# Kernel tuning notes

Measured on AMD Instinct MI355X. Metric: run time of the kernel, lower is better.

The kernel has to match this reference:

```python
import jax, jax.numpy as jnp
import numpy as np

N_NODES = 100000
N_EDGES = 1600000
N_GRAPHS = 4096
HID = 512
OUT_DIM = 12


def setup_inputs() -> dict:
    key = jax.random.key(0)
    ks = jax.random.split(key, 16)
    x = jax.random.normal(ks[0], (N_NODES, 7), dtype=jnp.float32)
    edge_index = jax.random.randint(ks[1], (2, N_EDGES), 0, N_NODES, dtype=jnp.int32)
    batch = jnp.sort(jax.random.randint(ks[2], (N_NODES,), 0, N_GRAPHS, dtype=jnp.int32))

    def lin(k, i, o):
        s = 1.0 / np.sqrt(i)
        kw, kb = jax.random.split(k)
        return (jax.random.uniform(kw, (i, o), jnp.float32, -s, s),
                jax.random.uniform(kb, (o,), jnp.float32, -s, s))

    c1_w1, c1_b1 = lin(ks[3], 7, HID)
    c1_w2, c1_b2 = lin(ks[4], HID, HID)
    c2_w1, c2_b1 = lin(ks[5], HID, HID)
    c2_w2, c2_b2 = lin(ks[6], HID, HID)
    c3_w1, c3_b1 = lin(ks[7], HID, HID)
    c3_w2, c3_b2 = lin(ks[8], HID, HID)
    lin_w1, lin_b1 = lin(ks[9], HID, 256)
    lin_w2, lin_b2 = lin(ks[10], 256, OUT_DIM)
    return dict(x=x, edge_index=edge_index, batch=batch,
                c1_w1=c1_w1, c1_b1=c1_b1, c1_w2=c1_w2, c1_b2=c1_b2,
                c2_w1=c2_w1, c2_b1=c2_b1, c2_w2=c2_w2, c2_b2=c2_b2,
                c3_w1=c3_w1, c3_b1=c3_b1, c3_w2=c3_w2, c3_b2=c3_b2,
                lin_w1=lin_w1, lin_b1=lin_b1, lin_w2=lin_w2, lin_b2=lin_b2)


def _gin_conv(x, src, dst, w1, b1, w2, b2):
    # GINConv (eps=0): h_i = mlp(x_i + sum_{j in N(i)} x_j)
    agg = jax.ops.segment_sum(x[src], dst, num_segments=N_NODES)
    h = x + agg
    h = jax.nn.relu(h @ w1 + b1) @ w2 + b2
    return h


def reference(x, edge_index, batch,
              c1_w1, c1_b1, c1_w2, c1_b2,
              c2_w1, c2_b1, c2_w2, c2_b2,
              c3_w1, c3_b1, c3_w2, c3_b2,
              lin_w1, lin_b1, lin_w2, lin_b2):
    src, dst = edge_index[0], edge_index[1]
    h = jax.nn.relu(_gin_conv(x, src, dst, c1_w1, c1_b1, c1_w2, c1_b2))
    h = jax.nn.relu(_gin_conv(h, src, dst, c2_w1, c2_b1, c2_w2, c2_b2))
    h = jax.nn.relu(_gin_conv(h, src, dst, c3_w1, c3_b1, c3_w2, c3_b2))
    # global mean pool over graphs in batch
    sums = jax.ops.segment_sum(h, batch, num_segments=N_GRAPHS)
    cnts = jax.ops.segment_sum(jnp.ones((h.shape[0],), h.dtype), batch, num_segments=N_GRAPHS)
    pooled = sums / jnp.maximum(cnts, 1.0)[:, None]
    return jax.nn.relu(pooled @ lin_w1 + lin_b1) @ lin_w2 + lin_b2
```

## Files before the change

kernel.cpp:

```cpp
#include <hip/hip_runtime.h>
#include <hip/hip_bf16.h>
#include <cstddef>
#include <cstdint>

#define N_NODES   100000
#define M_PAD     100096
#define N_EDGES   1600000
#define N_GRAPHS  4096
#define HID       512
#define OUT_DIM   12

typedef unsigned short u16;
typedef __attribute__((ext_vector_type(8))) short bf16x8;
typedef __attribute__((ext_vector_type(4))) float f32x4;

__device__ inline float bf2f(u16 u) {
    union { uint32_t i; float f; } v; v.i = (uint32_t)u << 16; return v.f;
}
__device__ inline u16 f2bf(float f) {
    union { float f; uint32_t i; } v; v.f = f;
    uint32_t r = v.i + 0x7FFFu + ((v.i >> 16) & 1u);
    return (u16)(r >> 16);
}

__device__ inline void load8_bf(const u16* p, float o[8]) {
    uint4 u = *(const uint4*)p;
    uint32_t w[4] = {u.x, u.y, u.z, u.w};
    #pragma unroll
    for (int i = 0; i < 4; ++i) {
        o[2*i]   = bf2f((u16)(w[i] & 0xFFFFu));
        o[2*i+1] = bf2f((u16)(w[i] >> 16));
    }
}
__device__ inline void store8_bf(u16* p, const float o[8]) {
    uint4 u;
    u.x = (uint32_t)f2bf(o[0]) | ((uint32_t)f2bf(o[1]) << 16);
    u.y = (uint32_t)f2bf(o[2]) | ((uint32_t)f2bf(o[3]) << 16);
    u.z = (uint32_t)f2bf(o[4]) | ((uint32_t)f2bf(o[5]) << 16);
    u.w = (uint32_t)f2bf(o[6]) | ((uint32_t)f2bf(o[7]) << 16);
    *(uint4*)p = u;
}

__device__ inline void gld16(const void* g, void* l) {
    __builtin_amdgcn_global_load_lds(
        (const __attribute__((address_space(1))) void*)g,
        (__attribute__((address_space(3))) void*)(uint32_t)(uintptr_t)l,
        16, 0, 0);
}

__global__ void zero_ints(int* __restrict__ p, int n) {
    int i = blockIdx.x * blockDim.x + threadIdx.x;
    if (i < n) p[i] = 0;
}

__global__ void hist_kernel(const int* __restrict__ dst, int* __restrict__ counts) {
    int e = blockIdx.x * blockDim.x + threadIdx.x;
    if (e < N_EDGES) atomicAdd(&counts[dst[e]], 1);
}

#define SCAN_NB 98

__global__ __launch_bounds__(1024) void scan_chunks(const int* __restrict__ counts,
                                                    int* __restrict__ row_start,
                                                    int* __restrict__ partials) {
    __shared__ int smem[1024];
    int tid = threadIdx.x;
    int i = blockIdx.x * 1024 + tid;
    int v = (i < N_NODES) ? counts[i] : 0;
    smem[tid] = v;
    __syncthreads();
    for (int off = 1; off < 1024; off <<= 1) {
        int t = (tid >= off) ? smem[tid - off] : 0;
        __syncthreads();
        smem[tid] += t;
        __syncthreads();
    }
    if (i < N_NODES) row_start[i + 1] = smem[tid];
    if (tid == 1023) partials[blockIdx.x] = smem[1023];
}

__global__ void scan_partials(int* __restrict__ partials) {
    if (threadIdx.x == 0 && blockIdx.x == 0) {
        int run = 0;
        for (int b = 0; b < SCAN_NB; ++b) {
            int t = partials[b];
            partials[b] = run;
            run += t;
        }
    }
}

__global__ __launch_bounds__(1024) void scan_add_offsets(int* __restrict__ row_start,
                                                         const int* __restrict__ partials) {
    int i = blockIdx.x * 1024 + threadIdx.x;
    if (i == 0) row_start[0] = 0;
    if (i < N_NODES) row_start[i + 1] += partials[blockIdx.x];
}

__global__ void cursor_init(const int* __restrict__ row_start, int* __restrict__ cursor) {
    int i = blockIdx.x * blockDim.x + threadIdx.x;
    if (i < N_NODES) cursor[i] = row_start[i];
}

__global__ void scatter_edges(const int* __restrict__ src, const int* __restrict__ dst,
                              int* __restrict__ cursor, int* __restrict__ sorted_src) {
    int e = blockIdx.x * blockDim.x + threadIdx.x;
    if (e < N_EDGES) {
        int p = atomicAdd(&cursor[dst[e]], 1);
        p = min(max(p, 0), N_EDGES - 1);
        sorted_src[p] = src[e];
    }
}

__global__ __launch_bounds__(256) void transpose_to_bf16(const float* __restrict__ W,
                                                         u16* __restrict__ Wt) {
    __shared__ float t[32][33];
    int bx = blockIdx.x * 32, by = blockIdx.y * 32;
    int tx = threadIdx.x & 31, ty = threadIdx.x >> 5;
    #pragma unroll
    for (int i = 0; i < 32; i += 8)
        t[ty + i][tx] = W[(size_t)(by + ty + i) * HID + bx + tx];
    __syncthreads();
    #pragma unroll
    for (int i = 0; i < 32; i += 8)
        Wt[(size_t)(bx + ty + i) * HID + by + tx] = f2bf(t[tx][ty + i]);
}

template <int HALF>
__global__ __launch_bounds__(256) void agg_half(const u16* __restrict__ X,
                                                const int* __restrict__ row_start,
                                                const int* __restrict__ sorted_src,
                                                u16* __restrict__ Out) {
    int node = blockIdx.x * 4 + (threadIdx.x >> 6);
    int lane = threadIdx.x & 63;
    size_t col = HALF * 256 + lane * 4;
    uint2 s = *(const uint2*)(X + (size_t)node * HID + col);
    float a0 = bf2f((u16)(s.x & 0xFFFFu)), a1 = bf2f((u16)(s.x >> 16));
    float a2 = bf2f((u16)(s.y & 0xFFFFu)), a3 = bf2f((u16)(s.y >> 16));
    int e0 = min(row_start[node], N_EDGES);
    int e1 = min(row_start[node + 1], N_EDGES);
    for (int e = e0; e < e1; ++e) {
        unsigned si = min((unsigned)sorted_src[e], (unsigned)(N_NODES - 1));
        uint2 v = *(const uint2*)(X + (size_t)si * HID + col);
        a0 += bf2f((u16)(v.x & 0xFFFFu)); a1 += bf2f((u16)(v.x >> 16));
        a2 += bf2f((u16)(v.y & 0xFFFFu)); a3 += bf2f((u16)(v.y >> 16));
    }
    uint2 o;
    o.x = (uint32_t)f2bf(a0) | ((uint32_t)f2bf(a1) << 16);
    o.y = (uint32_t)f2bf(a2) | ((uint32_t)f2bf(a3) << 16);
    unsigned long long packed = (unsigned long long)o.x | ((unsigned long long)o.y << 32);
    __builtin_nontemporal_store(packed,
        (unsigned long long*)(Out + (size_t)node * HID + col));
}

__global__ __launch_bounds__(64) void agg7_kernel(const float* __restrict__ x,
                                                  const int* __restrict__ row_start,
                                                  const int* __restrict__ sorted_src,
                                                  float* __restrict__ out) {
    int node = blockIdx.x * 8 + (threadIdx.x >> 3);
    int d = threadIdx.x & 7;
    if (node >= N_NODES || d >= 7) return;
    float acc = x[(size_t)node * 7 + d];
    int e0 = min(row_start[node], N_EDGES);
    int e1 = min(row_start[node + 1], N_EDGES);
    for (int e = e0; e < e1; ++e) {
        unsigned si = min((unsigned)sorted_src[e], (unsigned)(N_NODES - 1));
        acc += x[(size_t)si * 7 + d];
    }
    out[(size_t)node * 7 + d] = acc;
}

__global__ __launch_bounds__(256) void gemm_k7_relu(const float* __restrict__ A7,
                                                    const float* __restrict__ W,
                                                    const float* __restrict__ bias,
                                                    u16* __restrict__ C) {
    __shared__ float Wl[7 * HID];
    __shared__ float Bi[HID];
    __shared__ float A7l[128 * 7];
    int tid = threadIdx.x;
    int node0 = blockIdx.x * 128;
    for (int t = tid; t < 7 * HID; t += 256) Wl[t] = W[t];
    for (int t = tid; t < HID; t += 256) Bi[t] = bias[t];
    for (int t = tid; t < 128 * 7; t += 256) {
        int gi = node0 * 7 + t;
        A7l[t] = (gi < N_NODES * 7) ? A7[gi] : 0.f;
    }
    __syncthreads();
    int wid = tid >> 6, lane = tid & 63;
    for (int it = 0; it < 32; ++it) {
        int nl = it * 4 + wid;
        int node = node0 + nl;
        if (node >= N_NODES) break;
        float a[7];
        #pragma unroll
        for (int k = 0; k < 7; ++k) a[k] = A7l[nl * 7 + k];
        float s[8];
        int c0 = lane * 8;
        #pragma unroll
        for (int c = 0; c < 8; ++c) {
            float v = Bi[c0 + c];
            #pragma unroll
            for (int k = 0; k < 7; ++k) v = fmaf(a[k], Wl[k * HID + c0 + c], v);
            s[c] = fmaxf(v, 0.f);
        }
        store8_bf(C + (size_t)node * HID + c0, s);
    }
}

template <bool RELU>
__global__ __launch_bounds__(256) void gemm_mfma_bf16(const u16* __restrict__ A,
                                                      const u16* __restrict__ Wt,
                                                      const float* __restrict__ bias,
                                                      u16* __restrict__ C) {
    __shared__ u16 As[128][32];
    __shared__ u16 Bs[128][32];
    const int tid  = threadIdx.x;
    const int wid  = tid >> 6;
    const int lane = tid & 63;
    const int wr = wid >> 1, wc = wid & 1;
    const int row0 = blockIdx.y * 128;
    const int col0 = blockIdx.x * 128;
    const int l15 = lane & 15;
    const int l4  = lane >> 4;

    const int srow = lane >> 2;
    const int scol = (lane & 3) * 8;

    f32x4 acc[4][4] = {};

    for (int k0 = 0; k0 < HID; k0 += 32) {
        const u16* Ag = A  + (size_t)(row0 + wid * 32) * HID + k0;
        const u16* Bg = Wt + (size_t)(col0 + wid * 32) * HID + k0;
        #pragma unroll
        for (int i = 0; i < 2; ++i) {
            gld16(Ag + (size_t)(i * 16 + srow) * HID + scol, &As[wid * 32 + i * 16][0]);
            gld16(Bg + (size_t)(i * 16 + srow) * HID + scol, &Bs[wid * 32 + i * 16][0]);
        }
        __syncthreads();
        bf16x8 af[4], bfr[4];
        #pragma unroll
        for (int m = 0; m < 4; ++m)
            af[m] = *(const bf16x8*)&As[wr * 64 + m * 16 + l15][l4 * 8];
        #pragma unroll
        for (int n = 0; n < 4; ++n)
            bfr[n] = *(const bf16x8*)&Bs[wc * 64 + n * 16 + l15][l4 * 8];
        #pragma unroll
        for (int m = 0; m < 4; ++m)
            #pragma unroll
            for (int n = 0; n < 4; ++n)
                acc[m][n] = __builtin_amdgcn_mfma_f32_16x16x32_bf16(af[m], bfr[n],
                                                                    acc[m][n], 0, 0, 0);
        __syncthreads();
    }

    #pragma unroll
    for (int m = 0; m < 4; ++m) {
        #pragma unroll
        for (int n = 0; n < 4; ++n) {
            int col = col0 + wc * 64 + n * 16 + l15;
            float b = bias[col];
            #pragma unroll
            for (int i = 0; i < 4; ++i) {
                int r = row0 + wr * 64 + m * 16 + l4 * 4 + i;
                float v = acc[m][n][i] + b;
                if (RELU) v = fmaxf(v, 0.f);
                C[(size_t)r * HID + col] = f2bf(v);
            }
        }
    }
}

template <bool RELU>
__global__ __launch_bounds__(256) void gemm_tiled_f32(const float* __restrict__ A,
                                                      const float* __restrict__ W,
                                                      const float* __restrict__ bias,
                                                      float* __restrict__ C,
                                                      int M, int N, int K) {
    __shared__ float As[16][68];
    __shared__ float Bs[16][68];
    int tid = threadIdx.x;
    int tx = tid & 15, ty = tid >> 4;
    int col0 = blockIdx.x * 64;
    int row0 = blockIdx.y * 64;
    float acc[4][4] = {};

    for (int k0 = 0; k0 < K; k0 += 16) {
        {
            int r = tid >> 2, c = (tid & 3) * 4;
            float4 v = make_float4(0.f, 0.f, 0.f, 0.f);
            int gr = row0 + r;
            if (gr < M) v = *reinterpret_cast<const float4*>(A + (size_t)gr * K + k0 + c);
            As[c + 0][r] = v.x; As[c + 1][r] = v.y; As[c + 2][r] = v.z; As[c + 3][r] = v.w;
        }
        {
            int r = tid >> 4, c = (tid & 15) * 4;
            int gc = col0 + c;
            float4 v = make_float4(0.f, 0.f, 0.f, 0.f);
            const float* wp = W + (size_t)(k0 + r) * N + gc;
            if (gc + 3 < N) {
                v = *reinterpret_cast<const float4*>(wp);
            } else {
                float t0 = (gc + 0 < N) ? wp[0] : 0.f;
                float t1 = (gc + 1 < N) ? wp[1] : 0.f;
                float t2 = (gc + 2 < N) ? wp[2] : 0.f;
                v = make_float4(t0, t1, t2, 0.f);
            }
            *reinterpret_cast<float4*>(&Bs[r][c]) = v;
        }
        __syncthreads();
        #pragma unroll
        for (int k = 0; k < 16; ++k) {
            float a[4], b[4];
            *(float4*)a = *(const float4*)&As[k][ty * 4];
            *(float4*)b = *(const float4*)&Bs[k][tx * 4];
            #pragma unroll
            for (int i = 0; i < 4; ++i)
                #pragma unroll
                for (int j = 0; j < 4; ++j)
                    acc[i][j] = fmaf(a[i], b[j], acc[i][j]);
        }
        __syncthreads();
    }

    #pragma unroll
    for (int i = 0; i < 4; ++i) {
        int r = row0 + ty * 4 + i;
        if (r >= M) break;
        #pragma unroll
        for (int j = 0; j < 4; ++j) {
            int cidx = col0 + tx * 4 + j;
            if (cidx >= N) continue;
            float v = acc[i][j] + bias[cidx];
            if (RELU) v = fmaxf(v, 0.f);
            C[(size_t)r * N + cidx] = v;
        }
    }
}

__global__ void graph_bounds(const int* __restrict__ batch, int* __restrict__ g_start) {
    int g = blockIdx.x * blockDim.x + threadIdx.x;
    if (g > N_GRAPHS) return;
    int lo = 0, hi = N_NODES;
    while (lo < hi) {
        int mid = (lo + hi) >> 1;
        if (batch[mid] < g) lo = mid + 1; else hi = mid;
    }
    g_start[g] = lo;
}

__global__ __launch_bounds__(256) void pool_kernel(const u16* __restrict__ H,
                                                   const int* __restrict__ g_start,
                                                   float* __restrict__ pooled) {
    int g = blockIdx.x * 4 + (threadIdx.x >> 6);
    if (g >= N_GRAPHS) return;
    int lane = threadIdx.x & 63;
    int s = g_start[g], e = g_start[g + 1];
    float acc[8] = {};
    for (int n = s; n < e; ++n) {
        float v[8];
        load8_bf(H + (size_t)n * HID + lane * 8, v);
        #pragma unroll
        for (int k = 0; k < 8; ++k) acc[k] += v[k];
    }
    float inv = 1.f / fmaxf((float)(e - s), 1.f);
    float* o = pooled + (size_t)g * HID + lane * 8;
    #pragma unroll
    for (int k = 0; k < 8; ++k) o[k] = acc[k] * inv;
}

__global__ void diag_kernel(float* __restrict__ out, int n, float v) {
    int i = blockIdx.x * blockDim.x + threadIdx.x;
    if (i < n) out[i] = v;
}

static inline size_t rnd256(size_t b) { return (b + 255) & ~(size_t)255; }

extern "C" void kernel_launch(void* const* d_in, const int* in_sizes, int n_in,
                              void* d_out, int out_size, void* d_ws, size_t ws_size,
                              hipStream_t stream) {
    (void)in_sizes; (void)n_in;
    const float* x     = (const float*)d_in[0];
    const int*   ei    = (const int*)d_in[1];
    const int*   batch = (const int*)d_in[2];
    const int* src = ei;
    const int* dst = ei + N_EDGES;

    const float* c1_w1 = (const float*)d_in[3];
    const float* c1_b1 = (const float*)d_in[4];
    const float* c1_w2 = (const float*)d_in[5];
    const float* c1_b2 = (const float*)d_in[6];
    const float* c2_w1 = (const float*)d_in[7];
    const float* c2_b1 = (const float*)d_in[8];
    const float* c2_w2 = (const float*)d_in[9];
    const float* c2_b2 = (const float*)d_in[10];
    const float* c3_w1 = (const float*)d_in[11];
    const float* c3_b1 = (const float*)d_in[12];
    const float* c3_w2 = (const float*)d_in[13];
    const float* c3_b2 = (const float*)d_in[14];
    const float* lin_w1 = (const float*)d_in[15];
    const float* lin_b1 = (const float*)d_in[16];
    const float* lin_w2 = (const float*)d_in[17];
    const float* lin_b2 = (const float*)d_in[18];
    float* out = (float*)d_out;

    size_t off = 0;
    auto alloc = [&](size_t bytes) -> void* {
        void* p = (char*)d_ws + off;
        off += rnd256(bytes);
        return p;
    };
    u16*   b0        = (u16*)alloc((size_t)M_PAD * HID * 2);
    u16*   b1        = (u16*)alloc((size_t)M_PAD * HID * 2);
    float* agg7buf   = (float*)alloc((size_t)N_NODES * 7 * 4);
    int*   counts    = (int*)alloc((size_t)N_NODES * 4);
    int*   cursor    = (int*)alloc((size_t)N_NODES * 4);
    int*   row_start = (int*)alloc((size_t)(N_NODES + 1) * 4);
    int*   sorted_src= (int*)alloc((size_t)N_EDGES * 4);
    int*   g_start   = (int*)alloc((size_t)(N_GRAPHS + 1) * 4);
    int*   partials  = (int*)alloc((size_t)SCAN_NB * 4);
    float* pooled    = (float*)alloc((size_t)N_GRAPHS * HID * 4);
    char*  hh_slot   = (char*)alloc((size_t)N_GRAPHS * 256 * 4);
    float* hh        = (float*)hh_slot;
    u16*   wt        = (u16*)hh_slot;
    u16* c1w2T = wt + 0 * HID * HID;
    u16* c2w1T = wt + 1 * HID * HID;
    u16* c2w2T = wt + 2 * HID * HID;
    u16* c3w1T = wt + 3 * HID * HID;
    u16* c3w2T = wt + 4 * HID * HID;

    if (off > ws_size) {
        diag_kernel<<<(out_size + 255) / 256, 256, 0, stream>>>(
            out, out_size, (float)(ws_size >> 20));
        return;
    }

    zero_ints<<<(N_NODES + 255) / 256, 256, 0, stream>>>(counts, N_NODES);
    hist_kernel<<<(N_EDGES + 255) / 256, 256, 0, stream>>>(dst, counts);
    scan_chunks<<<SCAN_NB, 1024, 0, stream>>>(counts, row_start, partials);
    scan_partials<<<1, 64, 0, stream>>>(partials);
    scan_add_offsets<<<SCAN_NB, 1024, 0, stream>>>(row_start, partials);
    cursor_init<<<(N_NODES + 255) / 256, 256, 0, stream>>>(row_start, cursor);
    scatter_edges<<<(N_EDGES + 255) / 256, 256, 0, stream>>>(src, dst, cursor, sorted_src);
    graph_bounds<<<(N_GRAPHS + 256) / 256, 256, 0, stream>>>(batch, g_start);

    dim3 tgrid(HID / 32, HID / 32);
    transpose_to_bf16<<<tgrid, 256, 0, stream>>>(c1_w2, c1w2T);
    transpose_to_bf16<<<tgrid, 256, 0, stream>>>(c2_w1, c2w1T);
    transpose_to_bf16<<<tgrid, 256, 0, stream>>>(c2_w2, c2w2T);
    transpose_to_bf16<<<tgrid, 256, 0, stream>>>(c3_w1, c3w1T);
    transpose_to_bf16<<<tgrid, 256, 0, stream>>>(c3_w2, c3w2T);

    dim3 mgrid(HID / 128, M_PAD / 128);
    const int aggGrid = N_NODES / 4;

    agg7_kernel<<<(N_NODES + 7) / 8, 64, 0, stream>>>(x, row_start, sorted_src, agg7buf);
    gemm_k7_relu<<<(N_NODES + 127) / 128, 256, 0, stream>>>(agg7buf, c1_w1, c1_b1, b0);
    gemm_mfma_bf16<true><<<mgrid, 256, 0, stream>>>(b0, c1w2T, c1_b2, b1);
    agg_half<0><<<aggGrid, 256, 0, stream>>>(b1, row_start, sorted_src, b0);
    agg_half<1><<<aggGrid, 256, 0, stream>>>(b1, row_start, sorted_src, b0);
    gemm_mfma_bf16<true><<<mgrid, 256, 0, stream>>>(b0, c2w1T, c2_b1, b1);
    gemm_mfma_bf16<true><<<mgrid, 256, 0, stream>>>(b1, c2w2T, c2_b2, b0);
    agg_half<0><<<aggGrid, 256, 0, stream>>>(b0, row_start, sorted_src, b1);
    agg_half<1><<<aggGrid, 256, 0, stream>>>(b0, row_start, sorted_src, b1);
    gemm_mfma_bf16<true><<<mgrid, 256, 0, stream>>>(b1, c3w1T, c3_b1, b0);
    gemm_mfma_bf16<true><<<mgrid, 256, 0, stream>>>(b0, c3w2T, c3_b2, b1);
    pool_kernel<<<N_GRAPHS / 4, 256, 0, stream>>>(b1, g_start, pooled);
    gemm_tiled_f32<true><<<dim3(256 / 64, N_GRAPHS / 64), 256, 0, stream>>>(
        pooled, lin_w1, lin_b1, hh, N_GRAPHS, 256, HID);
    gemm_tiled_f32<false><<<dim3(1, N_GRAPHS / 64), 256, 0, stream>>>(
        hh, lin_w2, lin_b2, out, N_GRAPHS, OUT_DIM, 256);
}
```

Measured before the change: 1.613 ms.

## Double-buffer MFMA GEMM, stage epilogue via LDS, merge aggregation halves and transposes

The bf16 MFMA GEMM now double-buffers its A/B LDS tiles so the global-to-LDS load of the next K slice overlaps MFMA work on the current one. Its epilogue writes the tile to LDS first, then stores it to global memory as coalesced 16-byte rows. The two half-width neighbour aggregation kernels become one full-width kernel with 8 columns per lane, so each gathered source row is read in one pass. The five weight transposes become one launch with a z-dimension. The changes double GEMM LDS use, which may lower occupancy, and give the aggregation more registers per lane.

After: 1.448 ms. 1.11x faster.

```diff
diff --git a/kernel.cpp b/kernel.cpp
--- a/kernel.cpp
+++ b/kernel.cpp
@@ -39,6 +39,16 @@
     u.z = (uint32_t)f2bf(o[4]) | ((uint32_t)f2bf(o[5]) << 16);
     u.w = (uint32_t)f2bf(o[6]) | ((uint32_t)f2bf(o[7]) << 16);
     *(uint4*)p = u;
+}
+__device__ inline void store8_bf_nt(u16* p, const float o[8]) {
+    unsigned long long lo =
+        (unsigned long long)((uint32_t)f2bf(o[0]) | ((uint32_t)f2bf(o[1]) << 16)) |
+        ((unsigned long long)((uint32_t)f2bf(o[2]) | ((uint32_t)f2bf(o[3]) << 16)) << 32);
+    unsigned long long hi =
+        (unsigned long long)((uint32_t)f2bf(o[4]) | ((uint32_t)f2bf(o[5]) << 16)) |
+        ((unsigned long long)((uint32_t)f2bf(o[6]) | ((uint32_t)f2bf(o[7]) << 16)) << 32);
+    __builtin_nontemporal_store(lo, (unsigned long long*)p);
+    __builtin_nontemporal_store(hi, (unsigned long long*)(p + 4));
 }
 
 __device__ inline void gld16(const void* g, void* l) {
@@ -112,9 +122,16 @@
     }
 }
 
-__global__ __launch_bounds__(256) void transpose_to_bf16(const float* __restrict__ W,
-                                                         u16* __restrict__ Wt) {
+__global__ __launch_bounds__(256) void transpose5_to_bf16(const float* __restrict__ W0,
+                                                          const float* __restrict__ W1,
+                                                          const float* __restrict__ W2,
+                                                          const float* __restrict__ W3,
+                                                          const float* __restrict__ W4,
+                                                          u16* __restrict__ Wt) {
     __shared__ float t[32][33];
+    const float* Ws[5] = {W0, W1, W2, W3, W4};
+    const float* W = Ws[blockIdx.z];
+    u16* dst = Wt + (size_t)blockIdx.z * HID * HID;
     int bx = blockIdx.x * 32, by = blockIdx.y * 32;
     int tx = threadIdx.x & 31, ty = threadIdx.x >> 5;
     #pragma unroll
@@ -123,34 +140,28 @@
     __syncthreads();
     #pragma unroll
     for (int i = 0; i < 32; i += 8)
-        Wt[(size_t)(bx + ty + i) * HID + by + tx] = f2bf(t[tx][ty + i]);
-}
-
-template <int HALF>
-__global__ __launch_bounds__(256) void agg_half(const u16* __restrict__ X,
+        dst[(size_t)(bx + ty + i) * HID + by + tx] = f2bf(t[tx][ty + i]);
+}
+
+__global__ __launch_bounds__(256) void agg_full(const u16* __restrict__ X,
                                                 const int* __restrict__ row_start,
                                                 const int* __restrict__ sorted_src,
                                                 u16* __restrict__ Out) {
     int node = blockIdx.x * 4 + (threadIdx.x >> 6);
+    if (node >= N_NODES) return;
     int lane = threadIdx.x & 63;
-    size_t col = HALF * 256 + lane * 4;
-    uint2 s = *(const uint2*)(X + (size_t)node * HID + col);
-    float a0 = bf2f((u16)(s.x & 0xFFFFu)), a1 = bf2f((u16)(s.x >> 16));
-    float a2 = bf2f((u16)(s.y & 0xFFFFu)), a3 = bf2f((u16)(s.y >> 16));
+    float acc[8];
+    load8_bf(X + (size_t)node * HID + lane * 8, acc);
     int e0 = min(row_start[node], N_EDGES);
     int e1 = min(row_start[node + 1], N_EDGES);
     for (int e = e0; e < e1; ++e) {
         unsigned si = min((unsigned)sorted_src[e], (unsigned)(N_NODES - 1));
-        uint2 v = *(const uint2*)(X + (size_t)si * HID + col);
-        a0 += bf2f((u16)(v.x & 0xFFFFu)); a1 += bf2f((u16)(v.x >> 16));
-        a2 += bf2f((u16)(v.y & 0xFFFFu)); a3 += bf2f((u16)(v.y >> 16));
-    }
-    uint2 o;
-    o.x = (uint32_t)f2bf(a0) | ((uint32_t)f2bf(a1) << 16);
-    o.y = (uint32_t)f2bf(a2) | ((uint32_t)f2bf(a3) << 16);
-    unsigned long long packed = (unsigned long long)o.x | ((unsigned long long)o.y << 32);
-    __builtin_nontemporal_store(packed,
-        (unsigned long long*)(Out + (size_t)node * HID + col));
+        float v[8];
+        load8_bf(X + (size_t)si * HID + lane * 8, v);
+        #pragma unroll
+        for (int k = 0; k < 8; ++k) acc[k] += v[k];
+    }
+    store8_bf_nt(Out + (size_t)node * HID + lane * 8, acc);
 }
 
 __global__ __launch_bounds__(64) void agg7_kernel(const float* __restrict__ x,
@@ -212,8 +223,10 @@
                                                       const u16* __restrict__ Wt,
                                                       const float* __restrict__ bias,
                                                       u16* __restrict__ C) {
-    __shared__ u16 As[128][32];
-    __shared__ u16 Bs[128][32];
+    __shared__ u16 smem[2 * 2 * 128 * 32];
+    u16 (*As)[128][32] = (u16(*)[128][32])smem;
+    u16 (*Bs)[128][32] = (u16(*)[128][32])(smem + 2 * 128 * 32);
+
     const int tid  = threadIdx.x;
     const int wid  = tid >> 6;
     const int lane = tid & 63;
@@ -226,24 +239,33 @@
     const int srow = lane >> 2;
     const int scol = (lane & 3) * 8;
 
+    const u16* Ag0 = A  + (size_t)(row0 + wid * 32 + srow) * HID + scol;
+    const u16* Bg0 = Wt + (size_t)(col0 + wid * 32 + srow) * HID + scol;
+
+    auto stage = [&](int buf, int k0) {
+        #pragma unroll
+        for (int i = 0; i < 2; ++i) {
+            gld16(Ag0 + (size_t)i * 16 * HID + k0, &As[buf][wid * 32 + i * 16][0]);
+            gld16(Bg0 + (size_t)i * 16 * HID + k0, &Bs[buf][wid * 32 + i * 16][0]);
+        }
+    };
+
     f32x4 acc[4][4] = {};
 
-    for (int k0 = 0; k0 < HID; k0 += 32) {
-        const u16* Ag = A  + (size_t)(row0 + wid * 32) * HID + k0;
-        const u16* Bg = Wt + (size_t)(col0 + wid * 32) * HID + k0;
-        #pragma unroll
-        for (int i = 0; i < 2; ++i) {
-            gld16(Ag + (size_t)(i * 16 + srow) * HID + scol, &As[wid * 32 + i * 16][0]);
-            gld16(Bg + (size_t)(i * 16 + srow) * HID + scol, &Bs[wid * 32 + i * 16][0]);
-        }
-        __syncthreads();
+    stage(0, 0);
+    __syncthreads();
+
+    #pragma unroll 4
+    for (int kt = 0; kt < 16; ++kt) {
+        int cur = kt & 1;
+        if (kt < 15) stage(cur ^ 1, (kt + 1) * 32);
         bf16x8 af[4], bfr[4];
         #pragma unroll
         for (int m = 0; m < 4; ++m)
-            af[m] = *(const bf16x8*)&As[wr * 64 + m * 16 + l15][l4 * 8];
+            af[m] = *(const bf16x8*)&As[cur][wr * 64 + m * 16 + l15][l4 * 8];
         #pragma unroll
         for (int n = 0; n < 4; ++n)
-            bfr[n] = *(const bf16x8*)&Bs[wc * 64 + n * 16 + l15][l4 * 8];
+            bfr[n] = *(const bf16x8*)&Bs[cur][wc * 64 + n * 16 + l15][l4 * 8];
         #pragma unroll
         for (int m = 0; m < 4; ++m)
             #pragma unroll
@@ -253,20 +275,29 @@
         __syncthreads();
     }
 
+    u16* Ct = smem;
     #pragma unroll
     for (int m = 0; m < 4; ++m) {
         #pragma unroll
         for (int n = 0; n < 4; ++n) {
-            int col = col0 + wc * 64 + n * 16 + l15;
-            float b = bias[col];
+            int col = wc * 64 + n * 16 + l15;
+            float b = bias[col0 + col];
             #pragma unroll
             for (int i = 0; i < 4; ++i) {
-                int r = row0 + wr * 64 + m * 16 + l4 * 4 + i;
+                int r = wr * 64 + m * 16 + l4 * 4 + i;
                 float v = acc[m][n][i] + b;
                 if (RELU) v = fmaxf(v, 0.f);
-                C[(size_t)r * HID + col] = f2bf(v);
+                Ct[r * 128 + col] = f2bf(v);
             }
         }
+    }
+    __syncthreads();
+    #pragma unroll
+    for (int j = 0; j < 8; ++j) {
+        int c = tid + j * 256;
+        int r = c >> 4, cc = (c & 15) * 8;
+        uint4 v = *(const uint4*)&Ct[r * 128 + cc];
+        *(uint4*)&C[(size_t)(row0 + r) * HID + col0 + cc] = v;
     }
 }
 
@@ -442,13 +473,8 @@
     cursor_init<<<(N_NODES + 255) / 256, 256, 0, stream>>>(row_start, cursor);
     scatter_edges<<<(N_EDGES + 255) / 256, 256, 0, stream>>>(src, dst, cursor, sorted_src);
     graph_bounds<<<(N_GRAPHS + 256) / 256, 256, 0, stream>>>(batch, g_start);
-
-    dim3 tgrid(HID / 32, HID / 32);
-    transpose_to_bf16<<<tgrid, 256, 0, stream>>>(c1_w2, c1w2T);
-    transpose_to_bf16<<<tgrid, 256, 0, stream>>>(c2_w1, c2w1T);
-    transpose_to_bf16<<<tgrid, 256, 0, stream>>>(c2_w2, c2w2T);
-    transpose_to_bf16<<<tgrid, 256, 0, stream>>>(c3_w1, c3w1T);
-    transpose_to_bf16<<<tgrid, 256, 0, stream>>>(c3_w2, c3w2T);
+    transpose5_to_bf16<<<dim3(HID / 32, HID / 32, 5), 256, 0, stream>>>(
+        c1_w2, c2_w1, c2_w2, c3_w1, c3_w2, wt);
 
     dim3 mgrid(HID / 128, M_PAD / 128);
     const int aggGrid = N_NODES / 4;
@@ -456,12 +482,10 @@
     agg7_kernel<<<(N_NODES + 7) / 8, 64, 0, stream>>>(x, row_start, sorted_src, agg7buf);
     gemm_k7_relu<<<(N_NODES + 127) / 128, 256, 0, stream>>>(agg7buf, c1_w1, c1_b1, b0);
     gemm_mfma_bf16<true><<<mgrid, 256, 0, stream>>>(b0, c1w2T, c1_b2, b1);
-    agg_half<0><<<aggGrid, 256, 0, stream>>>(b1, row_start, sorted_src, b0);
-    agg_half<1><<<aggGrid, 256, 0, stream>>>(b1, row_start, sorted_src, b0);
+    agg_full<<<aggGrid, 256, 0, stream>>>(b1, row_start, sorted_src, b0);
     gemm_mfma_bf16<true><<<mgrid, 256, 0, stream>>>(b0, c2w1T, c2_b1, b1);
     gemm_mfma_bf16<true><<<mgrid, 256, 0, stream>>>(b1, c2w2T, c2_b2, b0);
-    agg_half<0><<<aggGrid, 256, 0, stream>>>(b0, row_start, sorted_src, b1);
-    agg_half<1><<<aggGrid, 256, 0, stream>>>(b0, row_start, sorted_src, b1);
+    agg_full<<<aggGrid, 256, 0, stream>>>(b0, row_start, sorted_src, b1);
     gemm_mfma_bf16<true><<<mgrid, 256, 0, stream>>>(b1, c3w1T, c3_b1, b0);
     gemm_mfma_bf16<true><<<mgrid, 256, 0, stream>>>(b0, c3w2T, c3_b2, b1);
     pool_kernel<<<N_GRAPHS / 4, 256, 0, stream>>>(b1, g_start, pooled);
```
